# Kernel optimization log

Measured on AMD Instinct MI355X. Metric: run time of the kernel, lower is better.

The kernel has to match this reference:

```python
import jax, jax.numpy as jnp
import numpy as np

NUM_BANDS, B, K, D = 5, 512, 64, 200
H = 4            # num attention heads
HID = 512        # selector hidden width
S = 0.02         # weight init scale


def setup_inputs() -> dict:
    key = jax.random.key(0)
    ks = jax.random.split(key, 8)
    F_IN = NUM_BANDS * K * D  # 64000
    return {
        "bands": jax.random.normal(ks[0], (NUM_BANDS, B, K, D), jnp.float32),
        "w1": jax.random.normal(ks[1], (HID, F_IN), jnp.float32) * S,
        "b1": jnp.zeros((HID,), jnp.float32),
        "w2": jax.random.normal(ks[2], (NUM_BANDS, HID), jnp.float32) * S,
        "b2": jnp.zeros((NUM_BANDS,), jnp.float32),
        "in_proj_w": jax.random.normal(ks[3], (3 * D, D), jnp.float32) * S,
        "in_proj_b": jnp.zeros((3 * D,), jnp.float32),
        "out_w": jax.random.normal(ks[4], (D, D), jnp.float32) * S,
        "out_b": jnp.zeros((D,), jnp.float32),
    }


def reference(bands, w1, b1, w2, b2, in_proj_w, in_proj_b, out_w, out_b):
    nb, Bb, k, d = bands.shape
    hd = d // H
    scale = 1.0 / np.sqrt(hd)

    # concat(bands, dim=1): [B, nb*k, d] in band-major order
    x = jnp.transpose(bands, (1, 0, 2, 3))           # [B, nb, k, d]
    kv_in = x.reshape(Bb, nb * k, d)                 # [B, nb*k, d]

    # router MLP + softmax + argmax band select
    flat = kv_in.reshape(Bb, -1)                     # [B, nb*k*d]
    h = jax.nn.relu(flat @ w1.T + b1)                # [B, HID]
    band_weights = jax.nn.softmax(h @ w2.T + b2, axis=-1)
    sel = jnp.argmax(band_weights, axis=-1)          # [B] int

    # gather selected band per sample as the query
    Q = bands[sel, jnp.arange(Bb)]                   # [B, k, d]

    # multihead cross-attention (torch nn.MultiheadAttention math)
    wq, wk, wv = jnp.split(in_proj_w, 3, axis=0)
    bq, bk, bv = jnp.split(in_proj_b, 3, axis=0)
    q = (Q @ wq.T + bq).reshape(Bb, k, H, hd).transpose(0, 2, 1, 3)        # [B,H,k,hd]
    kk = (kv_in @ wk.T + bk).reshape(Bb, nb * k, H, hd).transpose(0, 2, 1, 3)
    v = (kv_in @ wv.T + bv).reshape(Bb, nb * k, H, hd).transpose(0, 2, 1, 3)

    attn = jax.nn.softmax(jnp.einsum('bhqe,bhke->bhqk', q, kk) * scale, axis=-1)
    o = jnp.einsum('bhqk,bhke->bhqe', attn, v)       # [B,H,k,hd]
    o = o.transpose(0, 2, 1, 3).reshape(Bb, k, d)
    return o @ out_w.T + out_b                        # [B, k, d]
```

## Files before the change

kernel.cpp:

```cpp
#include <hip/hip_runtime.h>
#include <hip/hip_bf16.h>

#define NBANDS 5
#define BATCH  512
#define KQN    64
#define DM     200
#define NHEAD  4
#define HD     50
#define HIDW   512
#define TKV    320
#define FIN    64000
#define KSPLIT 20
#define KCH    3200
#define RCH    50
#define NTT    13
#define KST    7
#define NTKV   25
#define PLANE_ELEMS (KST * NTT * 64 * 8)

typedef __bf16  bf16x8 __attribute__((ext_vector_type(8)));
typedef float   f32x4  __attribute__((ext_vector_type(4)));

static __device__ inline unsigned short f2bf(float f) {
    __hip_bfloat16 h = __float2bfloat16(f);
    return *reinterpret_cast<unsigned short*>(&h);
}
static __device__ inline float bf2f(unsigned short u) {
    union { unsigned int i; float f; } x;
    x.i = ((unsigned int)u) << 16;
    return x.f;
}
static __device__ inline bf16x8 bf8zero() {
    union { bf16x8 v; unsigned int u[4]; } z;
    z.u[0] = z.u[1] = z.u[2] = z.u[3] = 0u;
    return z.v;
}
static __device__ inline void split8(const float4& a, const float4& b,
                                     bf16x8& hi, bf16x8& lo) {
    union { bf16x8 v; unsigned short u[8]; } H, L;
    const float xs[8] = {a.x, a.y, a.z, a.w, b.x, b.y, b.z, b.w};
#pragma unroll
    for (int i = 0; i < 8; ++i) {
        H.u[i] = f2bf(xs[i]);
        L.u[i] = f2bf(xs[i] - bf2f(H.u[i]));
    }
    hi = H.v; lo = L.v;
}
static __device__ inline bf16x8 round8(const float4& a, const float4& b) {
    union { bf16x8 v; unsigned short u[8]; } H;
    const float xs[8] = {a.x, a.y, a.z, a.w, b.x, b.y, b.z, b.w};
#pragma unroll
    for (int i = 0; i < 8; ++i) H.u[i] = f2bf(xs[i]);
    return H.v;
}

__global__ __launch_bounds__(256) void k_router_mfma(
    const float* __restrict__ bands, const float* __restrict__ w1,
    float* __restrict__ part)
{
    __shared__ __align__(16) unsigned short Ah[64][72];
    __shared__ __align__(16) unsigned short Al[64][72];
    __shared__ __align__(16) unsigned short Bh[64][72];
    __shared__ __align__(16) unsigned short Bl[64][72];

    const int lin     = (blockIdx.z << 6) + (blockIdx.y << 3) + blockIdx.x;
    const int logical = (lin & 7) * 160 + (lin >> 3);
    const int z   = logical >> 6;
    const int rem = logical & 63;
    const int j0  = (rem & 7) << 6;
    const int b0  = (rem >> 3) << 6;

    const int t  = threadIdx.x;
    const int w  = t >> 6, lane = t & 63;
    const int lm = lane & 15, quad = lane >> 4;
    const int m0 = w * 16;

    const int row0 = t >> 4, c4 = (t & 15) * 4;

    f32x4 acc[4];
#pragma unroll
    for (int nt = 0; nt < 4; ++nt) acc[nt] = (f32x4){0.f, 0.f, 0.f, 0.f};

    const int kbase = z * KCH;
    for (int chunk = 0; chunk < RCH; ++chunk) {
        const int kc = kbase + chunk * 64;
        const int band = kc / 12800;
        const float* abase = bands + (size_t)band * 6540800 + kc + c4;
        const float* bbase = w1 + (size_t)j0 * FIN + kc + c4;
        float4 av[4], bv[4];
#pragma unroll
        for (int r = 0; r < 4; ++r)
            av[r] = *(const float4*)(abase + (size_t)(b0 + row0 + r * 16) * 12800);
#pragma unroll
        for (int r = 0; r < 4; ++r)
            bv[r] = *(const float4*)(bbase + (size_t)(row0 + r * 16) * FIN);
        __syncthreads();
#pragma unroll
        for (int r = 0; r < 4; ++r) {
            const int row = row0 + r * 16;
            ushort4 hh, ll;
            hh.x = f2bf(av[r].x); ll.x = f2bf(av[r].x - bf2f(hh.x));
            hh.y = f2bf(av[r].y); ll.y = f2bf(av[r].y - bf2f(hh.y));
            hh.z = f2bf(av[r].z); ll.z = f2bf(av[r].z - bf2f(hh.z));
            hh.w = f2bf(av[r].w); ll.w = f2bf(av[r].w - bf2f(hh.w));
            *(ushort4*)&Ah[row][c4] = hh;
            *(ushort4*)&Al[row][c4] = ll;
        }
#pragma unroll
        for (int r = 0; r < 4; ++r) {
            const int row = row0 + r * 16;
            ushort4 hh, ll;
            hh.x = f2bf(bv[r].x); ll.x = f2bf(bv[r].x - bf2f(hh.x));
            hh.y = f2bf(bv[r].y); ll.y = f2bf(bv[r].y - bf2f(hh.y));
            hh.z = f2bf(bv[r].z); ll.z = f2bf(bv[r].z - bf2f(hh.z));
            hh.w = f2bf(bv[r].w); ll.w = f2bf(bv[r].w - bf2f(hh.w));
            *(ushort4*)&Bh[row][c4] = hh;
            *(ushort4*)&Bl[row][c4] = ll;
        }
        __syncthreads();
#pragma unroll
        for (int ks = 0; ks < 2; ++ks) {
            const int ka = ks * 32 + quad * 8;
            const bf16x8 a_h = *(const bf16x8*)&Ah[m0 + lm][ka];
            const bf16x8 a_l = *(const bf16x8*)&Al[m0 + lm][ka];
#pragma unroll
            for (int nt = 0; nt < 4; ++nt) {
                const bf16x8 b_h = *(const bf16x8*)&Bh[nt * 16 + lm][ka];
                const bf16x8 b_l = *(const bf16x8*)&Bl[nt * 16 + lm][ka];
                acc[nt] = __builtin_amdgcn_mfma_f32_16x16x32_bf16(a_h, b_h, acc[nt], 0, 0, 0);
                acc[nt] = __builtin_amdgcn_mfma_f32_16x16x32_bf16(a_l, b_h, acc[nt], 0, 0, 0);
                acc[nt] = __builtin_amdgcn_mfma_f32_16x16x32_bf16(a_h, b_l, acc[nt], 0, 0, 0);
            }
        }
    }
    float* po = part + (size_t)z * (BATCH * HIDW);
#pragma unroll
    for (int nt = 0; nt < 4; ++nt) {
        const int jj = j0 + nt * 16 + lm;
#pragma unroll
        for (int reg = 0; reg < 4; ++reg) {
            const int bb = b0 + m0 + quad * 4 + reg;
            po[(size_t)bb * HIDW + jj] = acc[nt][reg];
        }
    }
}

__global__ __launch_bounds__(256) void k_reduce_relu(
    const float* __restrict__ part, const float* __restrict__ b1,
    float* __restrict__ h)
{
    const int tid = blockIdx.x * 256 + threadIdx.x;
    float s = b1[tid & (HIDW - 1)];
#pragma unroll
    for (int z = 0; z < KSPLIT; ++z) s += part[z * (BATCH * HIDW) + tid];
    h[tid] = fmaxf(s, 0.f);
}

__global__ __launch_bounds__(256) void k_wpack(
    const float* __restrict__ ipw, const float* __restrict__ outw,
    unsigned short* __restrict__ WqHp, unsigned short* __restrict__ WqLp,
    unsigned short* __restrict__ OwHp, unsigned short* __restrict__ OwLp)
{
    const int p = blockIdx.x;
    const int ks = p / NTT, nt = p - ks * NTT;
    const int t = threadIdx.x;
    const int lane = t >> 2, e0 = (t & 3) * 2;
    const int lm = lane & 15, quad = lane >> 4;
    const int row = nt * 16 + lm;
    const int k  = ks * 32 + quad * 8 + e0;
    const float* src = (blockIdx.y == 0) ? ipw : outw;
    unsigned short* dh = (blockIdx.y == 0) ? WqHp : OwHp;
    unsigned short* dl = (blockIdx.y == 0) ? WqLp : OwLp;
    float v0 = 0.f, v1 = 0.f;
    if (row < DM && k < DM) {
        v0 = src[(size_t)row * DM + k];
        v1 = src[(size_t)row * DM + k + 1];
    }
    const int off = (p << 9) + (lane << 3) + e0;
    const unsigned short h0 = f2bf(v0), h1 = f2bf(v1);
    dh[off]     = h0;
    dh[off + 1] = h1;
    dl[off]     = f2bf(v0 - bf2f(h0));
    dl[off + 1] = f2bf(v1 - bf2f(h1));
}

__global__ __launch_bounds__(256) void k_wpack_kv(
    const float* __restrict__ ipw, unsigned short* __restrict__ Wkv)
{
    const int p = blockIdx.x;
    const int ks = p / NTKV, nt = p - ks * NTKV;
    const int t = threadIdx.x;
    const int lane = t >> 2, e0 = (t & 3) * 2;
    const int lm = lane & 15, quad = lane >> 4;
    const int row = nt * 16 + lm;
    const int k  = ks * 32 + quad * 8 + e0;
    float v0 = 0.f, v1 = 0.f;
    if (k < DM) {
        v0 = ipw[(size_t)(DM + row) * DM + k];
        v1 = ipw[(size_t)(DM + row) * DM + k + 1];
    }
    const int off = (p << 9) + (lane << 3) + e0;
    Wkv[off]     = f2bf(v0);
    Wkv[off + 1] = f2bf(v1);
}

__global__ __launch_bounds__(256) void k_argmax(
    const float* __restrict__ h, const float* __restrict__ w2,
    const float* __restrict__ b2, int* __restrict__ sel)
{
    __shared__ float red[NBANDS][256];
    const int b = blockIdx.x, t = threadIdx.x;
    float acc[NBANDS] = {0.f, 0.f, 0.f, 0.f, 0.f};
    for (int j = t; j < HIDW; j += 256) {
        const float hv = h[b * HIDW + j];
#pragma unroll
        for (int n = 0; n < NBANDS; ++n)
            acc[n] = fmaf(hv, w2[n * HIDW + j], acc[n]);
    }
#pragma unroll
    for (int n = 0; n < NBANDS; ++n) red[n][t] = acc[n];
    __syncthreads();
    for (int s = 128; s > 0; s >>= 1) {
        if (t < s) {
#pragma unroll
            for (int n = 0; n < NBANDS; ++n) red[n][t] += red[n][t + s];
        }
        __syncthreads();
    }
    if (t == 0) {
        int best = 0;
        float bv = red[0][0] + b2[0];
        for (int n = 1; n < NBANDS; ++n) {
            const float v = red[n][0] + b2[n];
            if (v > bv) { bv = v; best = n; }
        }
        sel[b] = best;
    }
}

template<bool BF16OUT>
static __device__ inline void proj_core(
    const float* __restrict__ x0,
    const unsigned short* __restrict__ Ph,
    const unsigned short* __restrict__ Pl,
    const float* __restrict__ bias,
    void* __restrict__ outp)
{
    const int t = threadIdx.x;
    const int w = t >> 6, lane = t & 63;
    const int lm = lane & 15, quad = lane >> 4;
    const int m0 = w * 16;
    const float* xrow = x0 + (size_t)(m0 + lm) * DM;

    f32x4 acc[NTT];
#pragma unroll
    for (int nt = 0; nt < NTT; ++nt) acc[nt] = (f32x4){0.f, 0.f, 0.f, 0.f};

#pragma unroll
    for (int ks = 0; ks < KST; ++ks) {
        const int k0 = ks * 32 + quad * 8;
        bf16x8 a_h = bf8zero(), a_l = bf8zero();
        if (k0 + 8 <= DM) {
            const float4 xa = *(const float4*)(xrow + k0);
            const float4 xb = *(const float4*)(xrow + k0 + 4);
            split8(xa, xb, a_h, a_l);
        }
        const unsigned short* ph = Ph + ((ks * NTT) << 9) + (lane << 3);
        const unsigned short* pl = Pl + ((ks * NTT) << 9) + (lane << 3);
#pragma unroll
        for (int nt = 0; nt < NTT; ++nt) {
            const bf16x8 b_h = *(const bf16x8*)(ph + (nt << 9));
            const bf16x8 b_l = *(const bf16x8*)(pl + (nt << 9));
            acc[nt] = __builtin_amdgcn_mfma_f32_16x16x32_bf16(a_h, b_h, acc[nt], 0, 0, 0);
            acc[nt] = __builtin_amdgcn_mfma_f32_16x16x32_bf16(a_l, b_h, acc[nt], 0, 0, 0);
            acc[nt] = __builtin_amdgcn_mfma_f32_16x16x32_bf16(a_h, b_l, acc[nt], 0, 0, 0);
        }
    }
#pragma unroll
    for (int nt = 0; nt < NTT; ++nt) {
        const int col = nt * 16 + lm;
        if (col < DM) {
            const float bs = bias[col];
#pragma unroll
            for (int reg = 0; reg < 4; ++reg) {
                const int row = m0 + quad * 4 + reg;
                const float v = acc[nt][reg] + bs;
                if (BF16OUT)
                    ((unsigned short*)outp)[(size_t)row * DM + col] = f2bf(v);
                else
                    ((float*)outp)[(size_t)row * DM + col] = v;
            }
        }
    }
}

__global__ __launch_bounds__(256) void k_qproj_mfma(
    const float* __restrict__ bands, const int* __restrict__ sel,
    const unsigned short* __restrict__ WqHp, const unsigned short* __restrict__ WqLp,
    const float* __restrict__ ipb, unsigned short* __restrict__ qb)
{
    const int b = blockIdx.x;
    const int band = sel[b];
    const float* x0 = bands + (size_t)((band * BATCH + b) * KQN) * DM;
    proj_core<true>(x0, WqHp, WqLp, ipb, qb + (size_t)(b * KQN) * DM);
}

__global__ __launch_bounds__(256) void k_outproj_mfma(
    const float* __restrict__ obuf, const unsigned short* __restrict__ OwHp,
    const unsigned short* __restrict__ OwLp, const float* __restrict__ outb,
    float* __restrict__ out)
{
    const int b = blockIdx.x;
    proj_core<false>(obuf + (size_t)(b * KQN) * DM, OwHp, OwLp, outb,
                     out + (size_t)(b * KQN) * DM);
}

__global__ __launch_bounds__(256) void k_kvproj_pk(
    const float* __restrict__ bands, const unsigned short* __restrict__ Wkv,
    const float* __restrict__ ipb, __hip_bfloat16* __restrict__ Kp,
    __hip_bfloat16* __restrict__ Vp)
{
    const int t = threadIdx.x;
    const int w = t >> 6, lane = t & 63;
    const int lm = lane & 15, quad = lane >> 4;
    const int m0 = w * 16;
    const int M0 = blockIdx.x * 64;

    const int gg = M0 + m0 + lm;
    const int bb = gg / TKV, tk = gg - bb * TKV;
    const int band = tk >> 6, kk = tk & 63;
    const float* xrow = bands + (size_t)((band * BATCH + bb) * KQN + kk) * DM;

    f32x4 acc[NTKV];
#pragma unroll
    for (int nt = 0; nt < NTKV; ++nt) acc[nt] = (f32x4){0.f, 0.f, 0.f, 0.f};

#pragma unroll
    for (int ks = 0; ks < KST; ++ks) {
        const int k0 = ks * 32 + quad * 8;
        bf16x8 a = bf8zero();
        if (k0 + 8 <= DM) {
            const float4 xa = *(const float4*)(xrow + k0);
            const float4 xb = *(const float4*)(xrow + k0 + 4);
            a = round8(xa, xb);
        }
        const unsigned short* pb = Wkv + ((ks * NTKV) << 9) + (lane << 3);
#pragma unroll
        for (int nt = 0; nt < NTKV; ++nt) {
            const bf16x8 b8 = *(const bf16x8*)(pb + (nt << 9));
            acc[nt] = __builtin_amdgcn_mfma_f32_16x16x32_bf16(a, b8, acc[nt], 0, 0, 0);
        }
    }
#pragma unroll
    for (int nt = 0; nt < NTKV; ++nt) {
        const int col = nt * 16 + lm;
        const float bias = ipb[DM + col];
#pragma unroll
        for (int reg = 0; reg < 4; ++reg) {
            const int grow = M0 + m0 + quad * 4 + reg;
            const float v = acc[nt][reg] + bias;
            if (col < DM) Kp[(size_t)grow * DM + col] = __float2bfloat16(v);
            else          Vp[(size_t)grow * DM + (col - DM)] = __float2bfloat16(v);
        }
    }
}

__global__ __launch_bounds__(256) void k_attn(
    const unsigned short* __restrict__ qb, const __hip_bfloat16* __restrict__ Kp,
    const __hip_bfloat16* __restrict__ Vp, float* __restrict__ obuf)
{
    __shared__ __align__(16) unsigned short Qs[64][72];
    __shared__ __align__(16) unsigned short KP[320][72];
    __shared__ __align__(16) unsigned short Vt[64][328];
    __shared__ __align__(16) unsigned short Ps[64][328];
    const int b = blockIdx.x, hh = blockIdx.y;
    const int t = threadIdx.x;

    const unsigned short* qbase = qb + (size_t)(b * KQN) * DM + hh * HD;
    for (int idx = t; idx < 64 * 64; idx += 256) {
        const int r = idx >> 6, e = idx & 63;
        Qs[r][e] = (e < HD) ? qbase[(size_t)r * DM + e] : 0;
    }
    const unsigned short* kbase = (const unsigned short*)Kp + (size_t)b * TKV * DM + hh * HD;
    for (int idx = t; idx < 320 * 25; idx += 256) {
        const int key = idx / 25, g = idx - key * 25;
        *(unsigned int*)&KP[key][g * 2] =
            *(const unsigned int*)(kbase + (size_t)key * DM + g * 2);
    }
    for (int idx = t; idx < 320 * 7; idx += 256) {
        const int key = idx / 7, g = idx - key * 7;
        *(unsigned int*)&KP[key][50 + g * 2] = 0;
    }
    const unsigned short* vbase = (const unsigned short*)Vp + (size_t)b * TKV * DM + hh * HD;
    for (int idx = t; idx < 320 * 25; idx += 256) {
        const int key = idx / 25, g = idx - key * 25;
        const unsigned int v = *(const unsigned int*)(vbase + (size_t)key * DM + g * 2);
        Vt[g * 2][key]     = (unsigned short)(v & 0xffffu);
        Vt[g * 2 + 1][key] = (unsigned short)(v >> 16);
    }
    __syncthreads();

    const int w = t >> 6, lane = t & 63;
    const int lm = lane & 15, quad = lane >> 4;
    const int m0 = w * 16;

    f32x4 s[20];
#pragma unroll
    for (int nt = 0; nt < 20; ++nt) s[nt] = (f32x4){0.f, 0.f, 0.f, 0.f};
#pragma unroll
    for (int ks = 0; ks < 2; ++ks) {
        const int ka = ks * 32 + quad * 8;
        const bf16x8 a = *(const bf16x8*)&Qs[m0 + lm][ka];
#pragma unroll
        for (int nt = 0; nt < 20; ++nt) {
            const bf16x8 bb8 = *(const bf16x8*)&KP[nt * 16 + lm][ka];
            s[nt] = __builtin_amdgcn_mfma_f32_16x16x32_bf16(a, bb8, s[nt], 0, 0, 0);
        }
    }

    const float scale = 0.14142135623730951f;
    float inv[4];
#pragma unroll
    for (int reg = 0; reg < 4; ++reg) {
        float mx = -1e30f;
#pragma unroll
        for (int nt = 0; nt < 20; ++nt) {
            const float sv = s[nt][reg] * scale;
            s[nt][reg] = sv;
            mx = fmaxf(mx, sv);
        }
#pragma unroll
        for (int off = 1; off < 16; off <<= 1)
            mx = fmaxf(mx, __shfl_xor(mx, off, 64));
        float lsum = 0.f;
#pragma unroll
        for (int nt = 0; nt < 20; ++nt) {
            const float p = __expf(s[nt][reg] - mx);
            s[nt][reg] = p;
            lsum += p;
        }
#pragma unroll
        for (int off = 1; off < 16; off <<= 1)
            lsum += __shfl_xor(lsum, off, 64);
        inv[reg] = 1.f / lsum;
    }
#pragma unroll
    for (int reg = 0; reg < 4; ++reg) {
        const int row = m0 + quad * 4 + reg;
#pragma unroll
        for (int nt = 0; nt < 20; ++nt)
            Ps[row][nt * 16 + lm] = f2bf(s[nt][reg]);
    }
    __syncthreads();

    f32x4 o[4];
#pragma unroll
    for (int nt = 0; nt < 4; ++nt) o[nt] = (f32x4){0.f, 0.f, 0.f, 0.f};
#pragma unroll
    for (int ks = 0; ks < 10; ++ks) {
        const int ka = ks * 32 + quad * 8;
        const bf16x8 a = *(const bf16x8*)&Ps[m0 + lm][ka];
#pragma unroll
        for (int nt = 0; nt < 4; ++nt) {
            const bf16x8 bb8 = *(const bf16x8*)&Vt[nt * 16 + lm][ka];
            o[nt] = __builtin_amdgcn_mfma_f32_16x16x32_bf16(a, bb8, o[nt], 0, 0, 0);
        }
    }
    float* op = obuf + (size_t)(b * KQN) * DM + hh * HD;
#pragma unroll
    for (int nt = 0; nt < 4; ++nt) {
        const int e = nt * 16 + lm;
        if (e < HD) {
#pragma unroll
            for (int reg = 0; reg < 4; ++reg) {
                const int row = m0 + quad * 4 + reg;
                op[(size_t)row * DM + e] = o[nt][reg] * inv[reg];
            }
        }
    }
}

extern "C" void kernel_launch(void* const* d_in, const int* in_sizes, int n_in,
                              void* d_out, int out_size, void* d_ws, size_t ws_size,
                              hipStream_t stream)
{
    const float* bands = (const float*)d_in[0];
    const float* w1    = (const float*)d_in[1];
    const float* b1    = (const float*)d_in[2];
    const float* w2    = (const float*)d_in[3];
    const float* b2    = (const float*)d_in[4];
    const float* ipw   = (const float*)d_in[5];
    const float* ipb   = (const float*)d_in[6];
    const float* outw  = (const float*)d_in[7];
    const float* outb  = (const float*)d_in[8];
    float* out = (float*)d_out;

    if (ws_size < (size_t)192940032) return;

    char* ws = (char*)d_ws;
    int*   sel  = (int*)  (ws + 0);
    float* part = (float*)(ws + 4096);
    float* h    = (float*)(ws + 20975616);
    unsigned short* qb = (unsigned short*)(ws + 4096);
    unsigned short* Wkv  = (unsigned short*)(ws + 26218496);
    unsigned short* WqHp = (unsigned short*)(ws + 26404096);
    unsigned short* WqLp = (unsigned short*)(ws + 26497280);
    unsigned short* OwHp = (unsigned short*)(ws + 26590464);
    unsigned short* OwLp = (unsigned short*)(ws + 26683648);
    __hip_bfloat16* Kp = (__hip_bfloat16*)(ws + 26776832);
    __hip_bfloat16* Vp = (__hip_bfloat16*)(ws + 92312832);
    float* obuf = (float*)(ws + 157848832);

    k_wpack_kv<<<KST * NTKV, 256, 0, stream>>>(ipw, Wkv);
    k_wpack<<<dim3(KST * NTT, 2), 256, 0, stream>>>(ipw, outw, WqHp, WqLp, OwHp, OwLp);

    k_router_mfma<<<dim3(8, 8, KSPLIT), 256, 0, stream>>>(bands, w1, part);
    k_reduce_relu<<<(BATCH * HIDW) / 256, 256, 0, stream>>>(part, b1, h);
    k_argmax<<<BATCH, 256, 0, stream>>>(h, w2, b2, sel);
    k_qproj_mfma<<<BATCH, 256, 0, stream>>>(bands, sel, WqHp, WqLp, ipb, qb);
    k_kvproj_pk<<<2560, 256, 0, stream>>>(bands, Wkv, ipb, Kp, Vp);
    k_attn<<<dim3(BATCH, NHEAD), 256, 0, stream>>>(qb, Kp, Vp, obuf);
    k_outproj_mfma<<<BATCH, 256, 0, stream>>>(obuf, OwHp, OwLp, outb, out);
}
```

Baseline: 941.9 us.

## Stage KV projection weights in LDS with double-buffered direct global-to-LDS loads

The KV projection kernel now copies each k-step's packed weight slab into a double-buffered shared-memory tile using global_load_lds, with barriers between steps. All four waves read the B fragments from LDS instead of each issuing redundant global loads. All activation rows are also loaded up front and converted to bf16 before the MFMA loop. This cuts repeated global or L2 traffic for the weights, at the cost of about 51KB of LDS per block, which may lower occupancy, and extra barriers.

```diff
diff --git a/kernel.cpp b/kernel.cpp
--- a/kernel.cpp
+++ b/kernel.cpp
@@ -16,7 +16,6 @@
 #define NTT    13
 #define KST    7
 #define NTKV   25
-#define PLANE_ELEMS (KST * NTT * 64 * 8)
 
 typedef __bf16  bf16x8 __attribute__((ext_vector_type(8)));
 typedef float   f32x4  __attribute__((ext_vector_type(4)));
@@ -315,11 +314,12 @@
                      out + (size_t)(b * KQN) * DM);
 }
 
-__global__ __launch_bounds__(256) void k_kvproj_pk(
+__global__ __launch_bounds__(256) void k_kvproj_lds(
     const float* __restrict__ bands, const unsigned short* __restrict__ Wkv,
     const float* __restrict__ ipb, __hip_bfloat16* __restrict__ Kp,
     __hip_bfloat16* __restrict__ Vp)
 {
+    __shared__ __align__(16) unsigned short Bs[2][NTKV * 512];
     const int t = threadIdx.x;
     const int w = t >> 6, lane = t & 63;
     const int lm = lane & 15, quad = lane >> 4;
@@ -331,26 +331,58 @@
     const int band = tk >> 6, kk = tk & 63;
     const float* xrow = bands + (size_t)((band * BATCH + bb) * KQN + kk) * DM;
 
-    f32x4 acc[NTKV];
-#pragma unroll
-    for (int nt = 0; nt < NTKV; ++nt) acc[nt] = (f32x4){0.f, 0.f, 0.f, 0.f};
-
+    float4 ar[2 * KST];
 #pragma unroll
     for (int ks = 0; ks < KST; ++ks) {
         const int k0 = ks * 32 + quad * 8;
-        bf16x8 a = bf8zero();
         if (k0 + 8 <= DM) {
-            const float4 xa = *(const float4*)(xrow + k0);
-            const float4 xb = *(const float4*)(xrow + k0 + 4);
-            a = round8(xa, xb);
-        }
-        const unsigned short* pb = Wkv + ((ks * NTKV) << 9) + (lane << 3);
+            ar[2 * ks]     = *(const float4*)(xrow + k0);
+            ar[2 * ks + 1] = *(const float4*)(xrow + k0 + 4);
+        }
+    }
+    bf16x8 a[KST];
+#pragma unroll
+    for (int ks = 0; ks < KST; ++ks) {
+        const int k0 = ks * 32 + quad * 8;
+        a[ks] = (k0 + 8 <= DM) ? round8(ar[2 * ks], ar[2 * ks + 1]) : bf8zero();
+    }
+
+    auto stage = [&](int ks, int buf) {
+        const unsigned short* src = Wkv + ((ks * NTKV) << 9);
+#pragma unroll
+        for (int pass = 0; pass < 6; ++pass) {
+            const int i = pass * 256 + t;
+            __builtin_amdgcn_global_load_lds(
+                (const __attribute__((address_space(1))) unsigned int*)(src + (size_t)i * 8),
+                (__attribute__((address_space(3))) unsigned int*)&Bs[buf][(pass * 256 + w * 64) * 8],
+                16, 0, 0);
+        }
+        if (t < 64) {
+            __builtin_amdgcn_global_load_lds(
+                (const __attribute__((address_space(1))) unsigned int*)(src + (size_t)(1536 + lane) * 8),
+                (__attribute__((address_space(3))) unsigned int*)&Bs[buf][1536 * 8],
+                16, 0, 0);
+        }
+    };
+
+    f32x4 acc[NTKV];
+#pragma unroll
+    for (int nt = 0; nt < NTKV; ++nt) acc[nt] = (f32x4){0.f, 0.f, 0.f, 0.f};
+
+    stage(0, 0);
+    __syncthreads();
+#pragma unroll
+    for (int ks = 0; ks < KST; ++ks) {
+        if (ks + 1 < KST) stage(ks + 1, (ks + 1) & 1);
+        const unsigned short* bs = &Bs[ks & 1][lane * 8];
 #pragma unroll
         for (int nt = 0; nt < NTKV; ++nt) {
-            const bf16x8 b8 = *(const bf16x8*)(pb + (nt << 9));
-            acc[nt] = __builtin_amdgcn_mfma_f32_16x16x32_bf16(a, b8, acc[nt], 0, 0, 0);
-        }
-    }
+            const bf16x8 b8 = *(const bf16x8*)(bs + (nt << 9));
+            acc[nt] = __builtin_amdgcn_mfma_f32_16x16x32_bf16(a[ks], b8, acc[nt], 0, 0, 0);
+        }
+        __syncthreads();
+    }
+
 #pragma unroll
     for (int nt = 0; nt < NTKV; ++nt) {
         const int col = nt * 16 + lm;
@@ -518,7 +550,7 @@
     k_reduce_relu<<<(BATCH * HIDW) / 256, 256, 0, stream>>>(part, b1, h);
     k_argmax<<<BATCH, 256, 0, stream>>>(h, w2, b2, sel);
     k_qproj_mfma<<<BATCH, 256, 0, stream>>>(bands, sel, WqHp, WqLp, ipb, qb);
-    k_kvproj_pk<<<2560, 256, 0, stream>>>(bands, Wkv, ipb, Kp, Vp);
+    k_kvproj_lds<<<2560, 256, 0, stream>>>(bands, Wkv, ipb, Kp, Vp);
     k_attn<<<dim3(BATCH, NHEAD), 256, 0, stream>>>(qb, Kp, Vp, obuf);
     k_outproj_mfma<<<BATCH, 256, 0, stream>>>(obuf, OwHp, OwLp, outb, out);
 }
```

New measurement: 782.8 us. -16.9%, faster.
